# Kernel tuning notes

Measured on AMD Instinct MI355X. Metric: run time of the kernel, lower is better.

## Reference

```python
import jax, jax.numpy as jnp
import numpy as np

BN_EPS = 1e-5
NN_EPS = 1e-8
K = 3


def conv_bn_relu(x, W, b, gamma, beta, mean, var):
    # x: [B, Cin, N]; W: [Cout, Cin] (1x1 conv); BN in inference mode w/ running stats
    y = jnp.einsum('bcn,oc->bon', x, W) + b[None, :, None]
    y = (y - mean[None, :, None]) * (gamma / jnp.sqrt(var + BN_EPS))[None, :, None] + beta[None, :, None]
    return jax.nn.relu(y)


def three_interpolation(p1, p2, f2):
    # p1: [B, N1, 3] unknown xyz; p2: [B, N2, 3] known xyz; f2: [B, C, N2]
    # squared pairwise distances via the expansion trick (avoids [B,N1,N2,3])
    d2 = (jnp.sum(p1 * p1, -1)[:, :, None]
          + jnp.sum(p2 * p2, -1)[:, None, :]
          - 2.0 * jnp.einsum('bnd,bmd->bnm', p1, p2))  # [B, N1, N2]
    neg_d2, idx = jax.lax.top_k(-d2, K)                 # 3 nearest
    dist = -neg_d2                                      # squared dists, [B, N1, 3]
    recip = 1.0 / (dist + NN_EPS)
    weight = recip / jnp.sum(recip, axis=-1, keepdims=True)  # [B, N1, 3]
    f2t = jnp.transpose(f2, (0, 2, 1))                  # [B, N2, C]
    gathered = jax.vmap(lambda f, i: f[i])(f2t, idx)    # [B, N1, 3, C]
    return jnp.einsum('bnkc,bnk->bcn', gathered, weight)  # [B, C, N1]


def setup_inputs() -> dict:
    key = jax.random.key(0)
    ks = jax.random.split(key, 16)
    B, N1, N2 = 8, 16384, 4096
    mlp = [256, 128, 128]
    inp = {
        'p1': jax.random.normal(ks[0], (B, N1, 3), jnp.float32),
        'p2': jax.random.normal(ks[1], (B, N2, 3), jnp.float32),
        'f2': jax.random.normal(ks[2], (B, mlp[0], N2), jnp.float32),
    }
    kidx = 3
    for li in range(len(mlp) - 1):
        cin, cout = mlp[li], mlp[li + 1]
        inp[f'W{li}'] = jax.random.normal(ks[kidx], (cout, cin), jnp.float32) * (1.0 / np.sqrt(cin)); kidx += 1
        inp[f'b{li}'] = jnp.zeros((cout,), jnp.float32)
        inp[f'gamma{li}'] = jnp.ones((cout,), jnp.float32)
        inp[f'beta{li}'] = jnp.zeros((cout,), jnp.float32)
        inp[f'mean{li}'] = jax.random.normal(ks[kidx], (cout,), jnp.float32) * 0.1; kidx += 1
        inp[f'var{li}'] = jax.random.uniform(ks[kidx], (cout,), jnp.float32, 0.5, 1.5); kidx += 1
    return inp


def reference(p1, p2, f2,
              W0, b0, gamma0, beta0, mean0, var0,
              W1, b1, gamma1, beta1, mean1, var1):
    f = conv_bn_relu(f2, W0, b0, gamma0, beta0, mean0, var0)
    f = conv_bn_relu(f, W1, b1, gamma1, beta1, mean1, var1)
    return three_interpolation(p1, p2, f)
```

## Files before the change

kernel.cpp:

```cpp
#include <hip/hip_runtime.h>

#define B_    8
#define N1_   16384
#define N2_   4096
#define NTOT_ (B_ * N1_)

__device__ __forceinline__ float np_sumsq(float x, float y, float z)
{
#pragma clang fp contract(off)
    return ((x * x + y * y) + z * z);
}

__global__ __launch_bounds__(256) void prep_kernel(
    const float* __restrict__ W0, const float* __restrict__ b0,
    const float* __restrict__ g0, const float* __restrict__ be0,
    const float* __restrict__ m0, const float* __restrict__ v0,
    const float* __restrict__ W1, const float* __restrict__ b1,
    const float* __restrict__ g1, const float* __restrict__ be1,
    const float* __restrict__ m1, const float* __restrict__ v1,
    const float* __restrict__ p2,
    float* __restrict__ W0p, float* __restrict__ b0p,
    float* __restrict__ W1p, float* __restrict__ b1p,
    float4* __restrict__ q4)
{
    const int bx = blockIdx.x;
    const int tid = threadIdx.x;
    if (bx < 128) {
        const int t = bx * 256 + tid;
        const int o = t >> 8;
        const float s = g0[o] / sqrtf(v0[o] + 1e-5f);
        W0p[t] = W0[t] * s;
        if (t < 128) {
            const float ss = g0[t] / sqrtf(v0[t] + 1e-5f);
            b0p[t] = be0[t] + (b0[t] - m0[t]) * ss;
        }
    } else if (bx < 192) {
        const int t = (bx - 128) * 256 + tid;
        const int o = t >> 7;
        const float s = g1[o] / sqrtf(v1[o] + 1e-5f);
        W1p[t] = W1[t] * s;
        if (t < 128) {
            const float ss = g1[t] / sqrtf(v1[t] + 1e-5f);
            b1p[t] = be1[t] + (b1[t] - m1[t]) * ss;
        }
    } else {
        const int t = (bx - 192) * 256 + tid;
        const float x = p2[3 * (size_t)t + 0];
        const float y = p2[3 * (size_t)t + 1];
        const float z = p2[3 * (size_t)t + 2];
        q4[t] = make_float4(x, y, z, np_sumsq(x, y, z));
    }
}

__global__ __launch_bounds__(256) void gemm_fused_kernel(
    const float* __restrict__ f2, const float* __restrict__ W0p,
    const float* __restrict__ b0p, const float* __restrict__ W1p,
    const float* __restrict__ b1p, float* __restrict__ f_t)
{
    __shared__ float A_lds[32][136];
    __shared__ float HT[128][132];
    float (*B_lds)[128] = (float(*)[128])&HT[0][0];

    const int b  = blockIdx.y;
    const int n0 = blockIdx.x * 128;
    const int tid = threadIdx.x;
    const int ty = tid >> 4;
    const int tx = tid & 15;

    float acc[8][8];

    const int a_kq = (tid & 7) * 4;
    const int a_r0 = tid >> 3;
    const int b_n4 = (tid & 31) * 4;
    const int b_k0 = tid >> 5;

#pragma unroll
    for (int i = 0; i < 8; ++i)
#pragma unroll
        for (int j = 0; j < 8; ++j) acc[i][j] = 0.f;

    {
        const float* Xb = f2 + (size_t)b * 256 * N2_;
        for (int k0 = 0; k0 < 256; k0 += 32) {
#pragma unroll
            for (int i = 0; i < 4; ++i) {
                const int row = a_r0 + 32 * i;
                const float4 v = *(const float4*)&W0p[(size_t)row * 256 + k0 + a_kq];
                A_lds[a_kq + 0][row] = v.x;
                A_lds[a_kq + 1][row] = v.y;
                A_lds[a_kq + 2][row] = v.z;
                A_lds[a_kq + 3][row] = v.w;
            }
#pragma unroll
            for (int i = 0; i < 4; ++i) {
                const int krow = b_k0 + 8 * i;
                *(float4*)&B_lds[krow][b_n4] =
                    *(const float4*)&Xb[(size_t)(k0 + krow) * N2_ + n0 + b_n4];
            }
            __syncthreads();

#pragma unroll
            for (int kk = 0; kk < 32; ++kk) {
                const float4 a0 = *(const float4*)&A_lds[kk][ty * 4];
                const float4 a1 = *(const float4*)&A_lds[kk][64 + ty * 4];
                const float4 bq0 = *(const float4*)&B_lds[kk][tx * 4];
                const float4 bq1 = *(const float4*)&B_lds[kk][64 + tx * 4];
                const float av[8] = {a0.x, a0.y, a0.z, a0.w, a1.x, a1.y, a1.z, a1.w};
                const float bv[8] = {bq0.x, bq0.y, bq0.z, bq0.w, bq1.x, bq1.y, bq1.z, bq1.w};
#pragma unroll
                for (int i = 0; i < 8; ++i)
#pragma unroll
                    for (int j = 0; j < 8; ++j)
                        acc[i][j] = fmaf(av[i], bv[j], acc[i][j]);
            }
            __syncthreads();
        }
    }

    {
        float bias_v[8];
#pragma unroll
        for (int i = 0; i < 8; ++i) {
            const int r = (i < 4) ? (ty * 4 + i) : (64 + ty * 4 + (i - 4));
            bias_v[i] = b0p[r];
        }
#pragma unroll
        for (int i = 0; i < 8; ++i) {
            const int r = (i < 4) ? (ty * 4 + i) : (64 + ty * 4 + (i - 4));
            float4 v0, v1;
            v0.x = fmaxf(acc[i][0] + bias_v[i], 0.f);
            v0.y = fmaxf(acc[i][1] + bias_v[i], 0.f);
            v0.z = fmaxf(acc[i][2] + bias_v[i], 0.f);
            v0.w = fmaxf(acc[i][3] + bias_v[i], 0.f);
            v1.x = fmaxf(acc[i][4] + bias_v[i], 0.f);
            v1.y = fmaxf(acc[i][5] + bias_v[i], 0.f);
            v1.z = fmaxf(acc[i][6] + bias_v[i], 0.f);
            v1.w = fmaxf(acc[i][7] + bias_v[i], 0.f);
            *(float4*)&HT[r][tx * 4] = v0;
            *(float4*)&HT[r][64 + tx * 4] = v1;
        }
    }

#pragma unroll
    for (int i = 0; i < 8; ++i)
#pragma unroll
        for (int j = 0; j < 8; ++j) acc[i][j] = 0.f;

    for (int k0 = 0; k0 < 128; k0 += 32) {
#pragma unroll
        for (int i = 0; i < 4; ++i) {
            const int row = a_r0 + 32 * i;
            const float4 v = *(const float4*)&W1p[(size_t)row * 128 + k0 + a_kq];
            A_lds[a_kq + 0][row] = v.x;
            A_lds[a_kq + 1][row] = v.y;
            A_lds[a_kq + 2][row] = v.z;
            A_lds[a_kq + 3][row] = v.w;
        }
        __syncthreads();

#pragma unroll
        for (int kk = 0; kk < 32; ++kk) {
            const float4 a0 = *(const float4*)&A_lds[kk][ty * 4];
            const float4 a1 = *(const float4*)&A_lds[kk][64 + ty * 4];
            const float4 bq0 = *(const float4*)&HT[k0 + kk][tx * 4];
            const float4 bq1 = *(const float4*)&HT[k0 + kk][64 + tx * 4];
            const float av[8] = {a0.x, a0.y, a0.z, a0.w, a1.x, a1.y, a1.z, a1.w};
            const float bv[8] = {bq0.x, bq0.y, bq0.z, bq0.w, bq1.x, bq1.y, bq1.z, bq1.w};
#pragma unroll
            for (int i = 0; i < 8; ++i)
#pragma unroll
                for (int j = 0; j < 8; ++j)
                    acc[i][j] = fmaf(av[i], bv[j], acc[i][j]);
        }
        __syncthreads();
    }

    {
        float bias_v[8];
#pragma unroll
        for (int i = 0; i < 8; ++i) {
            const int r = (i < 4) ? (ty * 4 + i) : (64 + ty * 4 + (i - 4));
            bias_v[i] = b1p[r];
        }
        float (*T)[132] = (float(*)[132])&A_lds[0][0];
#pragma unroll
        for (int s = 0; s < 4; ++s) {
            if ((tx >> 3) == (s & 1)) {
                const int joff = (s >> 1) * 4;
                const int cl0 = (tx & 7) * 4;
#pragma unroll
                for (int i = 0; i < 8; ++i) {
                    const int r = (i < 4) ? (ty * 4 + i) : (64 + ty * 4 + (i - 4));
#pragma unroll
                    for (int j = 0; j < 4; ++j)
                        T[cl0 + j][r] = fmaxf(acc[i][j + joff] + bias_v[i], 0.f);
                }
            }
            __syncthreads();
#pragma unroll
            for (int p = 0; p < 4; ++p) {
                const int row = (tid >> 5) + 8 * p;
                const float4 v = *(const float4*)&T[row][(tid & 31) * 4];
                float* orow = f_t + ((size_t)b * N2_ + n0 + 32 * s + row) * 128;
                *(float4*)&orow[(tid & 31) * 4] = v;
            }
            __syncthreads();
        }
    }
}

__global__ __launch_bounds__(256, 8) void knn_phase1(
    const float* __restrict__ p1, const float4* __restrict__ q4,
    float* __restrict__ part_d, int* __restrict__ part_i)
{
    __shared__ float4 qs[1024];
    const int tid = threadIdx.x;
    const int chunk = blockIdx.x & 3;
    const int g = (blockIdx.x >> 2) * 256 + tid;
    const int b = g >> 14;

    const float px = p1[3 * (size_t)g + 0];
    const float py = p1[3 * (size_t)g + 1];
    const float pz = p1[3 * (size_t)g + 2];
    const float s1 = np_sumsq(px, py, pz);

    const float4* qb = q4 + (size_t)b * N2_ + chunk * 1024;
#pragma unroll
    for (int i = 0; i < 4; ++i) qs[tid + i * 256] = qb[tid + i * 256];
    __syncthreads();

    float d0 = 1e30f, d1 = 1e30f, d2v = 1e30f;
    int i0 = 0, i1 = 0, i2 = 0;
    const int jbase = chunk * 1024;

    for (int j = 0; j < 1024; j += 4) {
#pragma unroll
        for (int u = 0; u < 4; ++u) {
            const float4 q = qs[j + u];
            const float dot = __fmaf_rn(px, q.x, __fmaf_rn(py, q.y, __fmul_rn(pz, q.z)));
            const float ss  = s1 + q.w;
            const float t   = __fmaf_rn(-2.0f, dot, ss);
            if (t < d2v) {
                const int jj = jbase + j + u;
                const bool c1 = t < d1, c0 = t < d0;
                d2v = c1 ? d1 : t;                 i2 = c1 ? i1 : jj;
                const float nd1 = c1 ? (c0 ? d0 : t) : d1;
                const int   ni1 = c1 ? (c0 ? i0 : jj) : i1;
                d1 = nd1;                          i1 = ni1;
                d0 = c0 ? t : d0;                  i0 = c0 ? jj : i0;
            }
        }
    }

    part_d[(0 * 4 + chunk) * NTOT_ + g] = d0;
    part_d[(1 * 4 + chunk) * NTOT_ + g] = d1;
    part_d[(2 * 4 + chunk) * NTOT_ + g] = d2v;
    part_i[(0 * 4 + chunk) * NTOT_ + g] = i0;
    part_i[(1 * 4 + chunk) * NTOT_ + g] = i1;
    part_i[(2 * 4 + chunk) * NTOT_ + g] = i2;
}

__global__ __launch_bounds__(256) void gather_kernel(
    const float* __restrict__ f_t, const float* __restrict__ part_d,
    const int* __restrict__ part_i, float* __restrict__ out)
{
    __shared__ float T[64][129];
    const int tid = threadIdx.x;
    const int lane = tid & 63, wv = tid >> 6;
    const int vb = (blockIdx.x & 7) * 256 + (blockIdx.x >> 3);
    const int gbase = vb * 64;
    const int g = gbase + lane;
    const int b = g >> 14, n0 = gbase & 16383;

    float d0 = 1e30f, d1 = 1e30f, d2v = 1e30f;
    int i0 = 0, i1 = 0, i2 = 0;
#pragma unroll
    for (int c = 0; c < 4; ++c) {
#pragma unroll
        for (int k = 0; k < 3; ++k) {
            const float t = part_d[(k * 4 + c) * NTOT_ + g];
            const int  jj = part_i[(k * 4 + c) * NTOT_ + g];
            if (t < d2v) {
                const bool c1 = t < d1, c0 = t < d0;
                d2v = c1 ? d1 : t;                 i2 = c1 ? i1 : jj;
                const float nd1 = c1 ? (c0 ? d0 : t) : d1;
                const int   ni1 = c1 ? (c0 ? i0 : jj) : i1;
                d1 = nd1;                          i1 = ni1;
                d0 = c0 ? t : d0;                  i0 = c0 ? jj : i0;
            }
        }
    }

    float w0, w1, w2;
    {
#pragma clang fp contract(off)
        const float r0 = 1.0f / (d0 + 1e-8f);
        const float r1 = 1.0f / (d1 + 1e-8f);
        const float r2 = 1.0f / (d2v + 1e-8f);
        const float rs = (r0 + r1) + r2;
        w0 = r0 / rs;
        w1 = r1 / rs;
        w2 = r2 / rs;
    }

    const float* fb = f_t + (size_t)b * N2_ * 128;
#pragma unroll
    for (int j = 0; j < 16; ++j) {
        const int q = wv * 16 + j;
        const int   qi0 = __shfl(i0, q);
        const int   qi1 = __shfl(i1, q);
        const int   qi2 = __shfl(i2, q);
        const float qw0 = __shfl(w0, q);
        const float qw1 = __shfl(w1, q);
        const float qw2 = __shfl(w2, q);
        const float2 a  = *(const float2*)(fb + (size_t)qi0 * 128 + 2 * lane);
        const float2 bb = *(const float2*)(fb + (size_t)qi1 * 128 + 2 * lane);
        const float2 c  = *(const float2*)(fb + (size_t)qi2 * 128 + 2 * lane);
        T[q][2 * lane + 0] = fmaf(qw0, a.x, fmaf(qw1, bb.x, qw2 * c.x));
        T[q][2 * lane + 1] = fmaf(qw0, a.y, fmaf(qw1, bb.y, qw2 * c.y));
    }
    __syncthreads();

    float* ob = out + ((size_t)b * 128) * N1_ + n0 + lane;
#pragma unroll
    for (int ci = 0; ci < 32; ++ci) {
        const int cch = wv * 32 + ci;
        __builtin_nontemporal_store(T[lane][cch], ob + (size_t)cch * N1_);
    }
}

extern "C" void kernel_launch(void* const* d_in, const int* in_sizes, int n_in,
                              void* d_out, int out_size, void* d_ws, size_t ws_size,
                              hipStream_t stream)
{
    const float* p1  = (const float*)d_in[0];
    const float* p2  = (const float*)d_in[1];
    const float* f2  = (const float*)d_in[2];
    const float* W0  = (const float*)d_in[3];
    const float* b0  = (const float*)d_in[4];
    const float* g0  = (const float*)d_in[5];
    const float* be0 = (const float*)d_in[6];
    const float* m0  = (const float*)d_in[7];
    const float* v0  = (const float*)d_in[8];
    const float* W1  = (const float*)d_in[9];
    const float* b1  = (const float*)d_in[10];
    const float* g1  = (const float*)d_in[11];
    const float* be1 = (const float*)d_in[12];
    const float* m1  = (const float*)d_in[13];
    const float* v1  = (const float*)d_in[14];

    char* ws = (char*)d_ws;
    float4* q4  = (float4*)(ws);
    float*  W0p = (float*)(ws + (512 << 10));
    float*  b0p = (float*)(ws + (640 << 10));
    float*  W1p = (float*)(ws + (644 << 10));
    float*  b1p = (float*)(ws + (708 << 10));
    float*  f_t = (float*)(ws + ((size_t)17 << 20));
    float*  pd  = (float*)(ws + ((size_t)1 << 20));
    int*    pi  = (int*)  (ws + ((size_t)9 << 20));

    prep_kernel<<<320, 256, 0, stream>>>(W0, b0, g0, be0, m0, v0,
                                         W1, b1, g1, be1, m1, v1,
                                         p2, W0p, b0p, W1p, b1p, q4);

    gemm_fused_kernel<<<dim3(32, 8), 256, 0, stream>>>(f2, W0p, b0p,
                                                       W1p, b1p, f_t);

    knn_phase1<<<(NTOT_ / 256) * 4, 256, 0, stream>>>(p1, q4, pd, pi);
    gather_kernel<<<NTOT_ / 64, 256, 0, stream>>>(f_t, pd, pi, (float*)d_out);
}
```

Measured before the change: 325.2 us.

## Fold BN prep and p2 packing into GEMM kernel; share gather weights via LDS

Removes the separate prep kernel launch by computing BN scales and biases inline in the fused GEMM kernel and adding extra blocks that pack p2 into float4. In the gather kernel only the first wavefront merges the partial top-3 results and computes weights, then broadcasts them to the other wavefronts through shared memory instead of every wave redoing the merge and using shuffles. This saves a launch and redundant partial-result loads, but the GEMM now recomputes sqrt/divides per block and the gather adds a block barrier.

```diff
diff --git a/kernel.cpp b/kernel.cpp
--- a/kernel.cpp
+++ b/kernel.cpp
@@ -11,59 +11,35 @@
     return ((x * x + y * y) + z * z);
 }
 
-__global__ __launch_bounds__(256) void prep_kernel(
+__global__ __launch_bounds__(256) void gemm_fused_kernel(
+    const float* __restrict__ f2,
     const float* __restrict__ W0, const float* __restrict__ b0,
     const float* __restrict__ g0, const float* __restrict__ be0,
     const float* __restrict__ m0, const float* __restrict__ v0,
     const float* __restrict__ W1, const float* __restrict__ b1,
     const float* __restrict__ g1, const float* __restrict__ be1,
     const float* __restrict__ m1, const float* __restrict__ v1,
-    const float* __restrict__ p2,
-    float* __restrict__ W0p, float* __restrict__ b0p,
-    float* __restrict__ W1p, float* __restrict__ b1p,
-    float4* __restrict__ q4)
-{
-    const int bx = blockIdx.x;
+    const float* __restrict__ p2, float4* __restrict__ q4,
+    float* __restrict__ f_t)
+{
+    __shared__ float A_lds[32][136];
+    __shared__ float HT[128][132];
+    float (*B_lds)[128] = (float(*)[128])&HT[0][0];
+
     const int tid = threadIdx.x;
-    if (bx < 128) {
-        const int t = bx * 256 + tid;
-        const int o = t >> 8;
-        const float s = g0[o] / sqrtf(v0[o] + 1e-5f);
-        W0p[t] = W0[t] * s;
-        if (t < 128) {
-            const float ss = g0[t] / sqrtf(v0[t] + 1e-5f);
-            b0p[t] = be0[t] + (b0[t] - m0[t]) * ss;
-        }
-    } else if (bx < 192) {
-        const int t = (bx - 128) * 256 + tid;
-        const int o = t >> 7;
-        const float s = g1[o] / sqrtf(v1[o] + 1e-5f);
-        W1p[t] = W1[t] * s;
-        if (t < 128) {
-            const float ss = g1[t] / sqrtf(v1[t] + 1e-5f);
-            b1p[t] = be1[t] + (b1[t] - m1[t]) * ss;
-        }
-    } else {
-        const int t = (bx - 192) * 256 + tid;
+    const int bx  = blockIdx.x;
+
+    if (bx >= 256) {
+        const int t = (bx - 256) * 256 + tid;
         const float x = p2[3 * (size_t)t + 0];
         const float y = p2[3 * (size_t)t + 1];
         const float z = p2[3 * (size_t)t + 2];
         q4[t] = make_float4(x, y, z, np_sumsq(x, y, z));
-    }
-}
-
-__global__ __launch_bounds__(256) void gemm_fused_kernel(
-    const float* __restrict__ f2, const float* __restrict__ W0p,
-    const float* __restrict__ b0p, const float* __restrict__ W1p,
-    const float* __restrict__ b1p, float* __restrict__ f_t)
-{
-    __shared__ float A_lds[32][136];
-    __shared__ float HT[128][132];
-    float (*B_lds)[128] = (float(*)[128])&HT[0][0];
-
-    const int b  = blockIdx.y;
-    const int n0 = blockIdx.x * 128;
-    const int tid = threadIdx.x;
+        return;
+    }
+
+    const int b  = bx >> 5;
+    const int n0 = (bx & 31) * 128;
     const int ty = tid >> 4;
     const int tx = tid & 15;
 
@@ -74,6 +50,14 @@
     const int b_n4 = (tid & 31) * 4;
     const int b_k0 = tid >> 5;
 
+    float s0w[4], s1w[4];
+#pragma unroll
+    for (int i = 0; i < 4; ++i) {
+        const int row = a_r0 + 32 * i;
+        s0w[i] = g0[row] / sqrtf(v0[row] + 1e-5f);
+        s1w[i] = g1[row] / sqrtf(v1[row] + 1e-5f);
+    }
+
 #pragma unroll
     for (int i = 0; i < 8; ++i)
 #pragma unroll
@@ -85,11 +69,12 @@
 #pragma unroll
             for (int i = 0; i < 4; ++i) {
                 const int row = a_r0 + 32 * i;
-                const float4 v = *(const float4*)&W0p[(size_t)row * 256 + k0 + a_kq];
-                A_lds[a_kq + 0][row] = v.x;
-                A_lds[a_kq + 1][row] = v.y;
-                A_lds[a_kq + 2][row] = v.z;
-                A_lds[a_kq + 3][row] = v.w;
+                const float4 v = *(const float4*)&W0[(size_t)row * 256 + k0 + a_kq];
+                const float s = s0w[i];
+                A_lds[a_kq + 0][row] = v.x * s;
+                A_lds[a_kq + 1][row] = v.y * s;
+                A_lds[a_kq + 2][row] = v.z * s;
+                A_lds[a_kq + 3][row] = v.w * s;
             }
 #pragma unroll
             for (int i = 0; i < 4; ++i) {
@@ -118,26 +103,22 @@
     }
 
     {
-        float bias_v[8];
 #pragma unroll
         for (int i = 0; i < 8; ++i) {
             const int r = (i < 4) ? (ty * 4 + i) : (64 + ty * 4 + (i - 4));
-            bias_v[i] = b0p[r];
-        }
-#pragma unroll
-        for (int i = 0; i < 8; ++i) {
-            const int r = (i < 4) ? (ty * 4 + i) : (64 + ty * 4 + (i - 4));
-            float4 v0, v1;
-            v0.x = fmaxf(acc[i][0] + bias_v[i], 0.f);
-            v0.y = fmaxf(acc[i][1] + bias_v[i], 0.f);
-            v0.z = fmaxf(acc[i][2] + bias_v[i], 0.f);
-            v0.w = fmaxf(acc[i][3] + bias_v[i], 0.f);
-            v1.x = fmaxf(acc[i][4] + bias_v[i], 0.f);
-            v1.y = fmaxf(acc[i][5] + bias_v[i], 0.f);
-            v1.z = fmaxf(acc[i][6] + bias_v[i], 0.f);
-            v1.w = fmaxf(acc[i][7] + bias_v[i], 0.f);
-            *(float4*)&HT[r][tx * 4] = v0;
-            *(float4*)&HT[r][64 + tx * 4] = v1;
+            const float s = g0[r] / sqrtf(v0[r] + 1e-5f);
+            const float bias_v = be0[r] + (b0[r] - m0[r]) * s;
+            float4 v0q, v1q;
+            v0q.x = fmaxf(acc[i][0] + bias_v, 0.f);
+            v0q.y = fmaxf(acc[i][1] + bias_v, 0.f);
+            v0q.z = fmaxf(acc[i][2] + bias_v, 0.f);
+            v0q.w = fmaxf(acc[i][3] + bias_v, 0.f);
+            v1q.x = fmaxf(acc[i][4] + bias_v, 0.f);
+            v1q.y = fmaxf(acc[i][5] + bias_v, 0.f);
+            v1q.z = fmaxf(acc[i][6] + bias_v, 0.f);
+            v1q.w = fmaxf(acc[i][7] + bias_v, 0.f);
+            *(float4*)&HT[r][tx * 4] = v0q;
+            *(float4*)&HT[r][64 + tx * 4] = v1q;
         }
     }
 
@@ -150,11 +131,12 @@
 #pragma unroll
         for (int i = 0; i < 4; ++i) {
             const int row = a_r0 + 32 * i;
-            const float4 v = *(const float4*)&W1p[(size_t)row * 128 + k0 + a_kq];
-            A_lds[a_kq + 0][row] = v.x;
-            A_lds[a_kq + 1][row] = v.y;
-            A_lds[a_kq + 2][row] = v.z;
-            A_lds[a_kq + 3][row] = v.w;
+            const float4 v = *(const float4*)&W1[(size_t)row * 128 + k0 + a_kq];
+            const float s = s1w[i];
+            A_lds[a_kq + 0][row] = v.x * s;
+            A_lds[a_kq + 1][row] = v.y * s;
+            A_lds[a_kq + 2][row] = v.z * s;
+            A_lds[a_kq + 3][row] = v.w * s;
         }
         __syncthreads();
 
@@ -180,7 +162,8 @@
 #pragma unroll
         for (int i = 0; i < 8; ++i) {
             const int r = (i < 4) ? (ty * 4 + i) : (64 + ty * 4 + (i - 4));
-            bias_v[i] = b1p[r];
+            const float s = g1[r] / sqrtf(v1[r] + 1e-5f);
+            bias_v[i] = be1[r] + (b1[r] - m1[r]) * s;
         }
         float (*T)[132] = (float(*)[132])&A_lds[0][0];
 #pragma unroll
@@ -265,54 +248,60 @@
     const int* __restrict__ part_i, float* __restrict__ out)
 {
     __shared__ float T[64][129];
+    __shared__ float mw[3][64];
+    __shared__ int   mi[3][64];
     const int tid = threadIdx.x;
     const int lane = tid & 63, wv = tid >> 6;
     const int vb = (blockIdx.x & 7) * 256 + (blockIdx.x >> 3);
     const int gbase = vb * 64;
-    const int g = gbase + lane;
-    const int b = g >> 14, n0 = gbase & 16383;
-
-    float d0 = 1e30f, d1 = 1e30f, d2v = 1e30f;
-    int i0 = 0, i1 = 0, i2 = 0;
-#pragma unroll
-    for (int c = 0; c < 4; ++c) {
-#pragma unroll
-        for (int k = 0; k < 3; ++k) {
-            const float t = part_d[(k * 4 + c) * NTOT_ + g];
-            const int  jj = part_i[(k * 4 + c) * NTOT_ + g];
-            if (t < d2v) {
-                const bool c1 = t < d1, c0 = t < d0;
-                d2v = c1 ? d1 : t;                 i2 = c1 ? i1 : jj;
-                const float nd1 = c1 ? (c0 ? d0 : t) : d1;
-                const int   ni1 = c1 ? (c0 ? i0 : jj) : i1;
-                d1 = nd1;                          i1 = ni1;
-                d0 = c0 ? t : d0;                  i0 = c0 ? jj : i0;
-            }
-        }
-    }
-
-    float w0, w1, w2;
-    {
+    const int b = gbase >> 14, n0 = gbase & 16383;
+
+    if (tid < 64) {
+        const int g = gbase + tid;
+        float d0 = 1e30f, d1 = 1e30f, d2v = 1e30f;
+        int i0 = 0, i1 = 0, i2 = 0;
+#pragma unroll
+        for (int c = 0; c < 4; ++c) {
+#pragma unroll
+            for (int k = 0; k < 3; ++k) {
+                const float t = part_d[(k * 4 + c) * NTOT_ + g];
+                const int  jj = part_i[(k * 4 + c) * NTOT_ + g];
+                if (t < d2v) {
+                    const bool c1 = t < d1, c0 = t < d0;
+                    d2v = c1 ? d1 : t;                 i2 = c1 ? i1 : jj;
+                    const float nd1 = c1 ? (c0 ? d0 : t) : d1;
+                    const int   ni1 = c1 ? (c0 ? i0 : jj) : i1;
+                    d1 = nd1;                          i1 = ni1;
+                    d0 = c0 ? t : d0;                  i0 = c0 ? jj : i0;
+                }
+            }
+        }
+        float w0, w1, w2;
+        {
 #pragma clang fp contract(off)
-        const float r0 = 1.0f / (d0 + 1e-8f);
-        const float r1 = 1.0f / (d1 + 1e-8f);
-        const float r2 = 1.0f / (d2v + 1e-8f);
-        const float rs = (r0 + r1) + r2;
-        w0 = r0 / rs;
-        w1 = r1 / rs;
-        w2 = r2 / rs;
-    }
+            const float r0 = 1.0f / (d0 + 1e-8f);
+            const float r1 = 1.0f / (d1 + 1e-8f);
+            const float r2 = 1.0f / (d2v + 1e-8f);
+            const float rs = (r0 + r1) + r2;
+            w0 = r0 / rs;
+            w1 = r1 / rs;
+            w2 = r2 / rs;
+        }
+        mw[0][tid] = w0;  mw[1][tid] = w1;  mw[2][tid] = w2;
+        mi[0][tid] = i0;  mi[1][tid] = i1;  mi[2][tid] = i2;
+    }
+    __syncthreads();
 
     const float* fb = f_t + (size_t)b * N2_ * 128;
 #pragma unroll
     for (int j = 0; j < 16; ++j) {
         const int q = wv * 16 + j;
-        const int   qi0 = __shfl(i0, q);
-        const int   qi1 = __shfl(i1, q);
-        const int   qi2 = __shfl(i2, q);
-        const float qw0 = __shfl(w0, q);
-        const float qw1 = __shfl(w1, q);
-        const float qw2 = __shfl(w2, q);
+        const int   qi0 = mi[0][q];
+        const int   qi1 = mi[1][q];
+        const int   qi2 = mi[2][q];
+        const float qw0 = mw[0][q];
+        const float qw1 = mw[1][q];
+        const float qw2 = mw[2][q];
         const float2 a  = *(const float2*)(fb + (size_t)qi0 * 128 + 2 * lane);
         const float2 bb = *(const float2*)(fb + (size_t)qi1 * 128 + 2 * lane);
         const float2 c  = *(const float2*)(fb + (size_t)qi2 * 128 + 2 * lane);
@@ -351,20 +340,14 @@
 
     char* ws = (char*)d_ws;
     float4* q4  = (float4*)(ws);
-    float*  W0p = (float*)(ws + (512 << 10));
-    float*  b0p = (float*)(ws + (640 << 10));
-    float*  W1p = (float*)(ws + (644 << 10));
-    float*  b1p = (float*)(ws + (708 << 10));
     float*  f_t = (float*)(ws + ((size_t)17 << 20));
     float*  pd  = (float*)(ws + ((size_t)1 << 20));
     int*    pi  = (int*)  (ws + ((size_t)9 << 20));
 
-    prep_kernel<<<320, 256, 0, stream>>>(W0, b0, g0, be0, m0, v0,
-                                         W1, b1, g1, be1, m1, v1,
-                                         p2, W0p, b0p, W1p, b1p, q4);
-
-    gemm_fused_kernel<<<dim3(32, 8), 256, 0, stream>>>(f2, W0p, b0p,
-                                                       W1p, b1p, f_t);
+    gemm_fused_kernel<<<384, 256, 0, stream>>>(f2,
+                                               W0, b0, g0, be0, m0, v0,
+                                               W1, b1, g1, be1, m1, v1,
+                                               p2, q4, f_t);
 
     knn_phase1<<<(NTOT_ / 256) * 4, 256, 0, stream>>>(p1, q4, pd, pi);
     gather_kernel<<<NTOT_ / 64, 256, 0, stream>>>(f_t, pd, pi, (float*)d_out);
```

Result: no change. 324.2 us (-0.3%).
